# Kernel optimization log

Hardware: AMD Instinct MI355X
Metric: run time of the kernel (lower is better)

The kernel has to match this reference:

```python
import jax, jax.numpy as jnp
import numpy as np

HID = 768
INTER = 3072
H = 12
DH = 64
N = 16384
W = 256   # attention_width
L = 512   # per-sequence length (power of 2, used via the uint32 bit-mask trick)


def rotate_every_two(x):
    x1 = x[..., ::2]
    x2 = x[..., 1::2]
    return jnp.stack((-x2, x1), axis=-1).reshape(x.shape)


def setup_inputs() -> dict:
    key = jax.random.key(0)
    ks = jax.random.split(key, 6)
    # GPT-J style interleaved rotary tables: sin/cos each value repeated twice
    inv_freq = 1.0 / (10000.0 ** (np.arange(0, DH, 2) / DH))  # [DH/2]
    ang = np.arange(N)[:, None] * inv_freq[None, :]           # [N, DH/2]
    pos_sin = jnp.asarray(np.repeat(np.sin(ang), 2, axis=-1), dtype=jnp.float32)
    pos_cos = jnp.asarray(np.repeat(np.cos(ang), 2, axis=-1), dtype=jnp.float32)
    return {
        "x": jax.random.normal(ks[0], (N, HID), dtype=jnp.float32),
        "normed_ages": jax.random.normal(ks[1], (N,), dtype=jnp.float32),
        "pos_sin": pos_sin,
        "pos_cos": pos_cos,
        "ln_scale": jnp.ones((HID,), dtype=jnp.float32),
        "ln_offset": jnp.zeros((HID,), dtype=jnp.float32),
        "w_in": jax.random.normal(ks[2], (HID, 3 * HID + INTER), dtype=jnp.float32) * 0.02,
        "b_in": jnp.zeros((3 * HID + INTER,), dtype=jnp.float32),
        "w_out": jax.random.normal(ks[3], (HID + INTER, HID), dtype=jnp.float32) * 0.02,
        "b_out": jnp.zeros((HID,), dtype=jnp.float32),
        "length": L,
    }


def reference(x, normed_ages, pos_sin, pos_cos, ln_scale, ln_offset,
              w_in, b_in, w_out, b_out, length):
    # LayerNorm (haiku: eps=1e-5, create_scale/offset)
    mu = jnp.mean(x, axis=-1, keepdims=True)
    var = jnp.var(x, axis=-1, keepdims=True)
    xn = (x - mu) * jax.lax.rsqrt(var + 1e-5) * ln_scale + ln_offset

    # fused QKV + FF projection (note: original computes x_with_ages but never uses it)
    mid = xn @ w_in + b_in
    q, k, v, ff = jnp.split(mid, [HID, 2 * HID, 3 * HID], axis=-1)

    def to_heads(t):  # [N, HID] -> [H, N, DH]
        return t.reshape(N, H, DH).transpose(1, 0, 2)

    q, k, v = to_heads(q), to_heads(k), to_heads(v)

    # rotary ('per_head'): sincos broadcast over heads
    sin, cos = pos_sin[None], pos_cos[None]
    q = q * cos + rotate_every_two(q) * sin
    k = k * cos + rotate_every_two(k) * sin

    # local (sliding-window, causal, within-sequence) attention, chunked by W
    C = W
    nc = N // C
    qc = q.reshape(H, nc, C, DH)
    kc = k.reshape(H, nc, C, DH)
    vc = v.reshape(H, nc, C, DH)
    kprev = jnp.concatenate([jnp.zeros_like(kc[:, :1]), kc[:, :-1]], axis=1)
    vprev = jnp.concatenate([jnp.zeros_like(vc[:, :1]), vc[:, :-1]], axis=1)
    kcat = jnp.concatenate([kprev, kc], axis=2)  # [H, nc, 2C, DH]
    vcat = jnp.concatenate([vprev, vc], axis=2)

    qi = (jnp.arange(nc) * C)[:, None] + jnp.arange(C)        # [nc, C]
    kj = (jnp.arange(nc) * C)[:, None] - C + jnp.arange(2 * C)  # [nc, 2C]
    lm = ~(jnp.uint32(length) - jnp.uint32(1))  # same bit-trick as the module
    same_seq = ((qi[:, :, None].astype(jnp.uint32) & lm) ==
                (jnp.maximum(kj, 0)[:, None, :].astype(jnp.uint32) & lm))
    d = qi[:, :, None] - kj[:, None, :]
    mask = (kj[:, None, :] >= 0) & (d >= 0) & (d < W) & same_seq  # [nc, C, 2C]

    scale = 1.0 / jnp.sqrt(jnp.float32(DH))
    scores = jnp.einsum('hncd,hnkd->hnck', qc, kcat) * scale
    scores = jnp.where(mask[None], scores, jnp.float32(-1e30))
    probs = jax.nn.softmax(scores, axis=-1)
    attn = jnp.einsum('hnck,hnkd->hncd', probs, vcat)

    attn = attn.reshape(H, N, DH).transpose(1, 0, 2).reshape(N, HID)
    combined = jnp.concatenate([attn, jax.nn.gelu(ff)], axis=-1)
    return xn + combined @ w_out + b_out
```

## Files before the change

kernel.cpp:

```cpp
#include <hip/hip_runtime.h>

#define N_TOK 16384
#define HIDN  768
#define MIDN  5376
#define COMBN 3840
#define NH    12
#define DHD   64
#define CHUNK 256
#define WIN   256

typedef short s16x8 __attribute__((ext_vector_type(8)));
typedef short s16x4 __attribute__((ext_vector_type(4)));
typedef float f32x4 __attribute__((ext_vector_type(4)));

__device__ __forceinline__ float bf2f(unsigned short u){
  union { unsigned u; float f; } x; x.u = ((unsigned)u) << 16; return x.f;
}
__device__ __forceinline__ unsigned short f2bf(float f){
  union { float f; unsigned u; } x; x.f = f;
  unsigned r = x.u + 0x7fffu + ((x.u >> 16) & 1u);
  return (unsigned short)(r >> 16);
}
__device__ __forceinline__ float gelu_fast(float x){
  float u = -1.5957691216057308f * (x + 0.044715f * x * x * x);
  return x / (1.f + __expf(u));
}
__device__ __forceinline__ void glds16(const void* g, void* l){
  __builtin_amdgcn_global_load_lds(
      (const __attribute__((address_space(1))) unsigned*)g,
      (__attribute__((address_space(3))) unsigned*)l, 16, 0, 0);
}

__global__ __launch_bounds__(256) void transpose_f2b(
    const float* __restrict__ in, unsigned short* __restrict__ out,
    int R, int Cc)
{
  __shared__ short t[64 * 72];
  const int tid = threadIdx.x;
  const int r0 = blockIdx.y * 64, c0 = blockIdx.x * 64;
  #pragma unroll
  for (int rep = 0; rep < 4; rep++){
    int v = tid + 256 * rep;
    int r = v >> 4, s = v & 15;
    float4 d = *(const float4*)(in + (size_t)(r0 + r) * Cc + c0 + s * 4);
    s16x4 o = { (short)f2bf(d.x), (short)f2bf(d.y), (short)f2bf(d.z), (short)f2bf(d.w) };
    *(s16x4*)(t + r * 72 + s * 4) = o;
  }
  __syncthreads();
  #pragma unroll
  for (int rep = 0; rep < 2; rep++){
    int v = tid + 256 * rep;
    int c = v & 63, s2 = v >> 6;
    s16x8 d;
    #pragma unroll
    for (int j = 0; j < 8; j++) d[j] = t[(s2 * 8 + j) * 72 + c];
    *(s16x8*)(out + (size_t)(c0 + c) * R + r0 + s2 * 8) = d;
  }
}

__global__ __launch_bounds__(256) void ln_kernel(
    const float* __restrict__ x, const float* __restrict__ sc,
    const float* __restrict__ ofs, unsigned short* __restrict__ xn)
{
  const int lane = threadIdx.x & 63, wv = threadIdx.x >> 6;
  const int row = blockIdx.x * 4 + wv;
  const float4* xr = (const float4*)(x + (size_t)row * HIDN);
  float4 vals[3];
  float sum = 0.f, sq = 0.f;
  #pragma unroll
  for (int j = 0; j < 3; j++){
    vals[j] = xr[lane + 64 * j];
    sum += vals[j].x + vals[j].y + vals[j].z + vals[j].w;
    sq  += vals[j].x * vals[j].x + vals[j].y * vals[j].y
         + vals[j].z * vals[j].z + vals[j].w * vals[j].w;
  }
  #pragma unroll
  for (int o = 1; o < 64; o <<= 1){ sum += __shfl_xor(sum, o); sq += __shfl_xor(sq, o); }
  const float mu = sum * (1.f / HIDN);
  const float rs = rsqrtf(fmaxf(sq * (1.f / HIDN) - mu * mu, 0.f) + 1e-5f);
  s16x4* xo = (s16x4*)(xn + (size_t)row * HIDN);
  const float4* scp = (const float4*)sc;
  const float4* ofp = (const float4*)ofs;
  #pragma unroll
  for (int j = 0; j < 3; j++){
    int p = lane + 64 * j;
    float4 s = scp[p], o = ofp[p];
    s16x4 w;
    w[0] = (short)f2bf((vals[j].x - mu) * rs * s.x + o.x);
    w[1] = (short)f2bf((vals[j].y - mu) * rs * s.y + o.y);
    w[2] = (short)f2bf((vals[j].z - mu) * rs * s.z + o.z);
    w[3] = (short)f2bf((vals[j].w - mu) * rs * s.w + o.w);
    xo[p] = w;
  }
}

template<int K>
__device__ __forceinline__ void gemm_pipe2(
    const unsigned short* __restrict__ A, const unsigned short* __restrict__ BT,
    short* SM,
    int tid, int quad, int l15, int wr, int wc, int m0, int n0,
    f32x4 acc[4][4])
{
  constexpr int T = K / 64;
  char* const SMc = (char*)SM;
  const int srow = tid >> 2;
  const int ksw  = ((tid & 3) ^ ((tid >> 3) & 3)) * 8;
  const unsigned short* Ap = A  + (size_t)(m0 + srow) * K + ksw;
  const unsigned short* Bp = BT + (size_t)(n0 + srow) * K + ksw;
  const size_t rstep = (size_t)64 * K;

  const int segx = ((quad ^ ((l15 >> 1) & 3)) << 4);
  int offA[4], offB[4];
  #pragma unroll
  for (int mf = 0; mf < 4; mf++) offA[mf] = (wr * 64 + mf * 16 + l15) * 64 + segx;
  #pragma unroll
  for (int nf = 0; nf < 4; nf++) offB[nf] = (wc * 64 + nf * 16 + l15) * 64 + segx;

  auto stage = [&](int tt, int kh, int b){
    const int coff = tt * 64 + kh * 32;
    char* Ad = SMc + b * 32768 + kh * 8192 + tid * 16;
    char* Bd = SMc + b * 32768 + 16384 + kh * 8192 + tid * 16;
    glds16(Ap + coff,         Ad);
    glds16(Ap + coff + rstep, Ad + 4096);
    glds16(Bp + coff,         Bd);
    glds16(Bp + coff + rstep, Bd + 4096);
  };

  s16x8 af[4], bf[4];
  auto rdfrags = [&](int b, int kh){
    const char* Ab = SMc + b * 32768 + kh * 8192;
    const char* Bb = SMc + b * 32768 + 16384 + kh * 8192;
    #pragma unroll
    for (int i = 0; i < 4; i++) af[i] = *(const s16x8*)(Ab + offA[i]);
    #pragma unroll
    for (int j = 0; j < 4; j++) bf[j] = *(const s16x8*)(Bb + offB[j]);
  };

  stage(0, 0, 0);
  stage(0, 1, 0);
  asm volatile("s_waitcnt vmcnt(4)" ::: "memory");
  asm volatile("s_barrier" ::: "memory");
  rdfrags(0, 0);

  for (int t = 0; t < T; ++t){
    const int cur = t & 1;
    if (t + 1 < T) stage(t + 1, 0, cur ^ 1);
    __builtin_amdgcn_s_setprio(1);
    #pragma unroll
    for (int i = 0; i < 4; i++)
      #pragma unroll
      for (int j = 0; j < 4; j++)
        acc[i][j] = __builtin_amdgcn_mfma_f32_16x16x32_bf16(af[i], bf[j], acc[i][j], 0, 0, 0);
    __builtin_amdgcn_s_setprio(0);
    if (t + 1 < T){ asm volatile("s_waitcnt vmcnt(4)" ::: "memory"); }
    else          { asm volatile("s_waitcnt vmcnt(0)" ::: "memory"); }
    asm volatile("s_barrier" ::: "memory");
    rdfrags(cur, 1);
    if (t + 1 < T) stage(t + 1, 1, cur ^ 1);
    __builtin_amdgcn_s_setprio(1);
    #pragma unroll
    for (int i = 0; i < 4; i++)
      #pragma unroll
      for (int j = 0; j < 4; j++)
        acc[i][j] = __builtin_amdgcn_mfma_f32_16x16x32_bf16(af[i], bf[j], acc[i][j], 0, 0, 0);
    __builtin_amdgcn_s_setprio(0);
    if (t + 1 < T){
      asm volatile("s_waitcnt vmcnt(4)" ::: "memory");
      asm volatile("s_barrier" ::: "memory");
      rdfrags(cur ^ 1, 0);
    }
  }
}

__global__ __launch_bounds__(256, 2) void gemm1_k(
    const unsigned short* __restrict__ A, const unsigned short* __restrict__ BT,
    const float* __restrict__ bias,
    unsigned short* __restrict__ qb, unsigned short* __restrict__ kb,
    unsigned short* __restrict__ vb, unsigned short* __restrict__ comb)
{
  __shared__ short SM[32768];
  const int tid = threadIdx.x, lane = tid & 63, wv = tid >> 6;
  const int quad = lane >> 4, l15 = lane & 15;
  const int wr = wv >> 1, wc = wv & 1;

  const int nbx = gridDim.x;
  const int bid = blockIdx.x + blockIdx.y * nbx;
  const int GM = 16;
  const int group = bid / (GM * nbx);
  const int rem   = bid % (GM * nbx);
  const int m0 = (group * GM + (rem % GM)) * 128;
  const int n0 = (rem / GM) * 128;

  f32x4 acc[4][4];
  #pragma unroll
  for (int i = 0; i < 4; i++)
    #pragma unroll
    for (int j = 0; j < 4; j++) acc[i][j] = (f32x4){0.f,0.f,0.f,0.f};

  gemm_pipe2<HIDN>(A, BT, SM, tid, quad, l15, wr, wc, m0, n0, acc);

  unsigned short* dstb; int cb; bool isff = false;
  if (n0 < 768)       { dstb = qb;   cb = n0; }
  else if (n0 < 1536) { dstb = kb;   cb = n0 - 768; }
  else if (n0 < 2304) { dstb = vb;   cb = n0 - 1536; }
  else                { dstb = comb; cb = n0 - 1536; isff = true; }
  const int rowstride = isff ? COMBN : HIDN;

  float bsv[4];
  #pragma unroll
  for (int nf = 0; nf < 4; nf++) bsv[nf] = bias[n0 + wc * 64 + nf * 16 + l15];

  #pragma unroll
  for (int mf = 0; mf < 4; mf++){
    #pragma unroll
    for (int r = 0; r < 4; r++){
      const int row = m0 + wr * 64 + mf * 16 + quad * 4 + r;
      unsigned short* rp = dstb + (size_t)row * rowstride + cb + wc * 64;
      #pragma unroll
      for (int nf = 0; nf < 4; nf++){
        float val = acc[mf][nf][r] + bsv[nf];
        if (isff) val = gelu_fast(val);
        rp[nf * 16 + l15] = f2bf(val);
      }
    }
  }
}

__global__ __launch_bounds__(256, 2) void gemm2_k(
    const unsigned short* __restrict__ A, const unsigned short* __restrict__ BT,
    const float* __restrict__ bias, const unsigned short* __restrict__ xn,
    float* __restrict__ outp)
{
  __shared__ short SM[32768];
  const int tid = threadIdx.x, lane = tid & 63, wv = tid >> 6;
  const int quad = lane >> 4, l15 = lane & 15;
  const int wr = wv >> 1, wc = wv & 1;
  const int n0 = blockIdx.x * 128, m0 = blockIdx.y * 128;

  f32x4 acc[4][4];
  #pragma unroll
  for (int i = 0; i < 4; i++)
    #pragma unroll
    for (int j = 0; j < 4; j++) acc[i][j] = (f32x4){0.f,0.f,0.f,0.f};

  gemm_pipe2<COMBN>(A, BT, SM, tid, quad, l15, wr, wc, m0, n0, acc);

  float bsv[4];
  #pragma unroll
  for (int nf = 0; nf < 4; nf++) bsv[nf] = bias[n0 + wc * 64 + nf * 16 + l15];

  #pragma unroll
  for (int mf = 0; mf < 4; mf++){
    #pragma unroll
    for (int r = 0; r < 4; r++){
      const int row = m0 + wr * 64 + mf * 16 + quad * 4 + r;
      const size_t rb = (size_t)row * HIDN + n0 + wc * 64;
      #pragma unroll
      for (int nf = 0; nf < 4; nf++){
        const size_t o = rb + nf * 16 + l15;
        outp[o] = bf2f(xn[o]) + acc[mf][nf][r] + bsv[nf];
      }
    }
  }
}

__global__ __launch_bounds__(384) void rope_qk(
    unsigned short* __restrict__ qb, unsigned short* __restrict__ kb,
    const float* __restrict__ psin, const float* __restrict__ pcos)
{
  __shared__ float ss[2048], cs[2048];
  const int tid = threadIdx.x, g = blockIdx.x;
  #pragma unroll
  for (int rep = 0; rep < 6; rep++){
    int idx = rep * 384 + tid;
    if (idx < 2048){
      int tok = idx >> 5, p = idx & 31;
      size_t gt = ((size_t)(g * 64 + tok)) * DHD + 2 * p;
      ss[idx] = psin[gt];
      cs[idx] = pcos[gt];
    }
  }
  __syncthreads();
  const int p = tid & 31;
  unsigned* q32 = (unsigned*)qb;
  unsigned* k32 = (unsigned*)kb;
  for (int tok = 0; tok < 64; tok++){
    const size_t a = ((size_t)(g * 64 + tok)) * 384 + tid;
    const float s = ss[tok * 32 + p], c0 = cs[tok * 32 + p];
    unsigned u = q32[a];
    float e = bf2f((unsigned short)(u & 0xffff));
    float d = bf2f((unsigned short)(u >> 16));
    q32[a] = (unsigned)f2bf((e * c0 - d * s) * 0.125f)
           | (((unsigned)f2bf((d * c0 + e * s) * 0.125f)) << 16);
    u = k32[a];
    e = bf2f((unsigned short)(u & 0xffff));
    d = bf2f((unsigned short)(u >> 16));
    k32[a] = (unsigned)f2bf(e * c0 - d * s)
           | (((unsigned)f2bf(d * c0 + e * s)) << 16);
  }
}

__global__ __launch_bounds__(256) void attn_kernel(
    const unsigned short* __restrict__ qb, const unsigned short* __restrict__ kb,
    const unsigned short* __restrict__ vb, unsigned short* __restrict__ comb,
    const int* __restrict__ lenp)
{
  __shared__ short Ks[2][64 * 72];
  __shared__ short Vt[2][64 * 64];
  __shared__ short Ps[4][16 * 72];
  const int tid = threadIdx.x, lane = tid & 63, wv = tid >> 6;
  const int quad = lane >> 4, l15 = lane & 15;
  const int h = blockIdx.y, c = blockIdx.x;
  const unsigned lm = ~((unsigned)lenp[0] - 1u);
  const int i0 = c * CHUNK + wv * 64;
  const unsigned short* qh = qb + h * DHD;
  const unsigned short* kh = kb + h * DHD;
  const unsigned short* vh = vb + h * DHD;

  s16x8 qf[4][2];
  #pragma unroll
  for (int rt = 0; rt < 4; rt++){
    const unsigned short* qr = qh + (size_t)(i0 + rt * 16 + l15) * HIDN;
    qf[rt][0] = *(const s16x8*)(qr + quad * 8);
    qf[rt][1] = *(const s16x8*)(qr + 32 + quad * 8);
  }

  f32x4 O[4][4];
  float mm[4][4], ll[4][4];
  #pragma unroll
  for (int rt = 0; rt < 4; rt++)
    #pragma unroll
    for (int j = 0; j < 4; j++){ O[rt][j] = (f32x4){0,0,0,0}; mm[rt][j] = -1e30f; ll[rt][j] = 0.f; }
  short* myP = &Ps[wv][0];

  const int skey = tid & 63, sseg = tid >> 6;
  const int jb0 = c * CHUNK - 256;
  s16x8 kr[2], vr[2];

  auto issue = [&](int jb){
    if (jb >= 0){
      const unsigned short* kp = kh + (size_t)(jb + skey) * HIDN + sseg * 16;
      const unsigned short* vp = vh + (size_t)(jb + skey) * HIDN + sseg * 16;
      kr[0] = *(const s16x8*)(kp);     kr[1] = *(const s16x8*)(kp + 8);
      vr[0] = *(const s16x8*)(vp);     vr[1] = *(const s16x8*)(vp + 8);
    } else {
      kr[0] = kr[1] = vr[0] = vr[1] = (s16x8){0,0,0,0,0,0,0,0};
    }
  };

  issue(jb0);
  for (int tb = 0; tb < 8; tb++){
    const int jb = jb0 + tb * 64;
    const int buf = tb & 1;
    short* Kb = &Ks[buf][0];
    short* Vb = &Vt[buf][0];
    *(s16x8*)(Kb + skey * 72 + sseg * 16)     = kr[0];
    *(s16x8*)(Kb + skey * 72 + sseg * 16 + 8) = kr[1];
    #pragma unroll
    for (int half = 0; half < 2; half++)
      #pragma unroll
      for (int j = 0; j < 8; j++){
        const int d = sseg * 16 + half * 8 + j;
        Vb[d * 64 + (((skey & 56) ^ ((d & 7) << 3)) | (skey & 7))] = vr[half][j];
      }
    if (tb < 7) issue(jb + 64);
    __syncthreads();

    const bool act = (jb >= 0) && (jb <= i0 + 63) && (jb + 63 >= i0 - 255) &&
                     (((unsigned)i0 & lm) == ((unsigned)jb & lm));
    if (!act) continue;

    #pragma unroll
    for (int rt = 0; rt < 4; rt++){
      const int ilo = i0 + rt * 16;
      if (ilo + 15 < jb || ilo - (jb + 63) >= WIN) continue;
      f32x4 sc[4];
      #pragma unroll
      for (int ct = 0; ct < 4; ct++){
        const short* kbase = Kb + (ct * 16 + l15) * 72 + quad * 8;
        const s16x8 b0 = *(const s16x8*)(kbase);
        const s16x8 b1 = *(const s16x8*)(kbase + 32);
        f32x4 aa = (f32x4){0,0,0,0};
        aa = __builtin_amdgcn_mfma_f32_16x16x32_bf16(qf[rt][0], b0, aa, 0, 0, 0);
        aa = __builtin_amdgcn_mfma_f32_16x16x32_bf16(qf[rt][1], b1, aa, 0, 0, 0);
        sc[ct] = aa;
      }
      float alph[4];
      #pragma unroll
      for (int r = 0; r < 4; r++){
        const int i = ilo + quad * 4 + r;
        #pragma unroll
        for (int ct = 0; ct < 4; ct++){
          const unsigned dd = (unsigned)(i - (jb + ct * 16 + l15));
          if (dd >= 256u) sc[ct][r] = -1e30f;
        }
        float mx = fmaxf(fmaxf(sc[0][r], sc[1][r]), fmaxf(sc[2][r], sc[3][r]));
        mx = fmaxf(mx, __shfl_xor(mx, 1));
        mx = fmaxf(mx, __shfl_xor(mx, 2));
        mx = fmaxf(mx, __shfl_xor(mx, 4));
        mx = fmaxf(mx, __shfl_xor(mx, 8));
        const float mnew = fmaxf(mm[rt][r], mx);
        alph[r] = __expf(mm[rt][r] - mnew);
        mm[rt][r] = mnew;
        float p0 = __expf(sc[0][r] - mnew);
        float p1 = __expf(sc[1][r] - mnew);
        float p2 = __expf(sc[2][r] - mnew);
        float p3 = __expf(sc[3][r] - mnew);
        sc[0][r] = p0; sc[1][r] = p1; sc[2][r] = p2; sc[3][r] = p3;
        float rsum = (p0 + p1) + (p2 + p3);
        rsum += __shfl_xor(rsum, 1);
        rsum += __shfl_xor(rsum, 2);
        rsum += __shfl_xor(rsum, 4);
        rsum += __shfl_xor(rsum, 8);
        ll[rt][r] = ll[rt][r] * alph[r] + rsum;
      }
      #pragma unroll
      for (int co = 0; co < 4; co++)
        #pragma unroll
        for (int r = 0; r < 4; r++) O[rt][co][r] *= alph[r];
      #pragma unroll
      for (int r = 0; r < 4; r++){
        const int prow = quad * 4 + r;
        #pragma unroll
        for (int ct = 0; ct < 4; ct++)
          myP[prow * 72 + ct * 16 + l15] = (short)f2bf(sc[ct][r]);
      }
      #pragma unroll
      for (int ks2 = 0; ks2 < 2; ks2++){
        const s16x8 pf = *(const s16x8*)(myP + l15 * 72 + ks2 * 32 + quad * 8);
        #pragma unroll
        for (int co = 0; co < 4; co++){
          const int d = co * 16 + l15;
          const s16x8 vf = *(const s16x8*)(Vb + d * 64 +
                              ((ks2 * 32 + quad * 8) ^ ((d & 7) << 3)));
          O[rt][co] = __builtin_amdgcn_mfma_f32_16x16x32_bf16(pf, vf, O[rt][co], 0, 0, 0);
        }
      }
    }
  }

  #pragma unroll
  for (int rt = 0; rt < 4; rt++)
    #pragma unroll
    for (int co = 0; co < 4; co++)
      #pragma unroll
      for (int r = 0; r < 4; r++){
        const int tok = i0 + rt * 16 + quad * 4 + r;
        comb[(size_t)tok * COMBN + h * DHD + co * 16 + l15] = f2bf(O[rt][co][r] / ll[rt][r]);
      }
}

extern "C" void kernel_launch(void* const* d_in, const int* in_sizes, int n_in,
                              void* d_out, int out_size, void* d_ws, size_t ws_size,
                              hipStream_t stream)
{
  const float* x     = (const float*)d_in[0];
  const float* psin  = (const float*)d_in[2];
  const float* pcos  = (const float*)d_in[3];
  const float* lns   = (const float*)d_in[4];
  const float* lno   = (const float*)d_in[5];
  const float* w_in  = (const float*)d_in[6];
  const float* b_in  = (const float*)d_in[7];
  const float* w_out = (const float*)d_in[8];
  const float* b_out = (const float*)d_in[9];
  const int*   lenp  = (const int*)d_in[10];
  float* out = (float*)d_out;

  char* ws = (char*)d_ws;
  size_t off = 0;
  unsigned short* xn    = (unsigned short*)(ws + off); off += (size_t)N_TOK * HIDN * 2;
  unsigned short* wInT  = (unsigned short*)(ws + off); off += (size_t)MIDN * HIDN * 2;
  unsigned short* wOutT = (unsigned short*)(ws + off); off += (size_t)HIDN * COMBN * 2;
  unsigned short* qbuf  = (unsigned short*)(ws + off); off += (size_t)N_TOK * HIDN * 2;
  unsigned short* kbuf  = (unsigned short*)(ws + off); off += (size_t)N_TOK * HIDN * 2;
  unsigned short* vbuf  = (unsigned short*)(ws + off); off += (size_t)N_TOK * HIDN * 2;
  unsigned short* comb  = (unsigned short*)(ws + off); off += (size_t)N_TOK * COMBN * 2;

  transpose_f2b<<<dim3(MIDN/64, HIDN/64), 256, 0, stream>>>(w_in, wInT, HIDN, MIDN);
  transpose_f2b<<<dim3(HIDN/64, COMBN/64), 256, 0, stream>>>(w_out, wOutT, COMBN, HIDN);
  ln_kernel<<<dim3(N_TOK/4), 256, 0, stream>>>(x, lns, lno, xn);
  gemm1_k<<<dim3(MIDN/128, N_TOK/128), 256, 0, stream>>>(
      xn, wInT, b_in, qbuf, kbuf, vbuf, comb);
  rope_qk<<<dim3(N_TOK/64), 384, 0, stream>>>(qbuf, kbuf, psin, pcos);
  attn_kernel<<<dim3(N_TOK/CHUNK, NH), 256, 0, stream>>>(
      qbuf, kbuf, vbuf, comb, lenp);
  gemm2_k<<<dim3(HIDN/128, N_TOK/128), 256, 0, stream>>>(
      comb, wOutT, b_out, xn, out);
}
```

Before: 613.7 us.

## Fuse rotary embedding into QKV GEMM epilogue and remap tiles per XCD

The rotary embedding and the query scaling now run inside the first GEMM's epilogue, using a lane shuffle to fetch each pair partner. This removes the separate rope kernel and its extra read and write pass over the q and k buffers. The block-to-tile mapping also changes so that consecutive block IDs (round-robin across the 8 XCDs) land on a contiguous group of M tiles per XCD, aiming for better L2 reuse. The epilogue now reads sin/cos tables directly from global memory, which adds some load traffic and register pressure.

```diff
diff --git a/kernel.cpp b/kernel.cpp
--- a/kernel.cpp
+++ b/kernel.cpp
@@ -175,6 +175,7 @@
 __global__ __launch_bounds__(256, 2) void gemm1_k(
     const unsigned short* __restrict__ A, const unsigned short* __restrict__ BT,
     const float* __restrict__ bias,
+    const float* __restrict__ psin, const float* __restrict__ pcos,
     unsigned short* __restrict__ qb, unsigned short* __restrict__ kb,
     unsigned short* __restrict__ vb, unsigned short* __restrict__ comb)
 {
@@ -183,13 +184,10 @@
   const int quad = lane >> 4, l15 = lane & 15;
   const int wr = wv >> 1, wc = wv & 1;
 
-  const int nbx = gridDim.x;
-  const int bid = blockIdx.x + blockIdx.y * nbx;
-  const int GM = 16;
-  const int group = bid / (GM * nbx);
-  const int rem   = bid % (GM * nbx);
-  const int m0 = (group * GM + (rem % GM)) * 128;
-  const int n0 = (rem / GM) * 128;
+  const int p = blockIdx.x + blockIdx.y * gridDim.x;
+  const int xcd = p & 7, slot = p >> 3;
+  const int m0 = (xcd * 16 + (slot & 15)) * 128;
+  const int n0 = (slot >> 4) * 128;
 
   f32x4 acc[4][4];
   #pragma unroll
@@ -199,28 +197,51 @@
 
   gemm_pipe2<HIDN>(A, BT, SM, tid, quad, l15, wr, wc, m0, n0, acc);
 
-  unsigned short* dstb; int cb; bool isff = false;
-  if (n0 < 768)       { dstb = qb;   cb = n0; }
-  else if (n0 < 1536) { dstb = kb;   cb = n0 - 768; }
-  else if (n0 < 2304) { dstb = vb;   cb = n0 - 1536; }
-  else                { dstb = comb; cb = n0 - 1536; isff = true; }
-  const int rowstride = isff ? COMBN : HIDN;
+  unsigned short* dstb; int cb; int cls;
+  if (n0 < 768)       { dstb = qb;   cb = n0;        cls = 0; }
+  else if (n0 < 1536) { dstb = kb;   cb = n0 - 768;  cls = 1; }
+  else if (n0 < 2304) { dstb = vb;   cb = n0 - 1536; cls = 2; }
+  else                { dstb = comb; cb = n0 - 1536; cls = 3; }
+  const int rowstride = (cls == 3) ? COMBN : HIDN;
 
   float bsv[4];
   #pragma unroll
   for (int nf = 0; nf < 4; nf++) bsv[nf] = bias[n0 + wc * 64 + nf * 16 + l15];
 
-  #pragma unroll
-  for (int mf = 0; mf < 4; mf++){
-    #pragma unroll
-    for (int r = 0; r < 4; r++){
-      const int row = m0 + wr * 64 + mf * 16 + quad * 4 + r;
-      unsigned short* rp = dstb + (size_t)row * rowstride + cb + wc * 64;
-      #pragma unroll
-      for (int nf = 0; nf < 4; nf++){
-        float val = acc[mf][nf][r] + bsv[nf];
-        if (isff) val = gelu_fast(val);
-        rp[nf * 16 + l15] = f2bf(val);
+  if (cls <= 1){
+    const float qscale = (cls == 0) ? 0.125f : 1.0f;
+    #pragma unroll
+    for (int mf = 0; mf < 4; mf++){
+      #pragma unroll
+      for (int r = 0; r < 4; r++){
+        const int row = m0 + wr * 64 + mf * 16 + quad * 4 + r;
+        unsigned short* rp = dstb + (size_t)row * rowstride + cb + wc * 64;
+        const float* sp = psin + (size_t)row * DHD;
+        const float* cp = pcos + (size_t)row * DHD;
+        #pragma unroll
+        for (int nf = 0; nf < 4; nf++){
+          const int d = nf * 16 + l15;
+          float v = acc[mf][nf][r] + bsv[nf];
+          float vp = __shfl_xor(v, 1);
+          const float s = sp[d], c = cp[d];
+          float o = (l15 & 1) ? (v * c + vp * s) : (v * c - vp * s);
+          rp[d] = f2bf(o * qscale);
+        }
+      }
+    }
+  } else {
+    #pragma unroll
+    for (int mf = 0; mf < 4; mf++){
+      #pragma unroll
+      for (int r = 0; r < 4; r++){
+        const int row = m0 + wr * 64 + mf * 16 + quad * 4 + r;
+        unsigned short* rp = dstb + (size_t)row * rowstride + cb + wc * 64;
+        #pragma unroll
+        for (int nf = 0; nf < 4; nf++){
+          float val = acc[mf][nf][r] + bsv[nf];
+          if (cls == 3) val = gelu_fast(val);
+          rp[nf * 16 + l15] = f2bf(val);
+        }
       }
     }
   }
@@ -261,42 +282,6 @@
         outp[o] = bf2f(xn[o]) + acc[mf][nf][r] + bsv[nf];
       }
     }
-  }
-}
-
-__global__ __launch_bounds__(384) void rope_qk(
-    unsigned short* __restrict__ qb, unsigned short* __restrict__ kb,
-    const float* __restrict__ psin, const float* __restrict__ pcos)
-{
-  __shared__ float ss[2048], cs[2048];
-  const int tid = threadIdx.x, g = blockIdx.x;
-  #pragma unroll
-  for (int rep = 0; rep < 6; rep++){
-    int idx = rep * 384 + tid;
-    if (idx < 2048){
-      int tok = idx >> 5, p = idx & 31;
-      size_t gt = ((size_t)(g * 64 + tok)) * DHD + 2 * p;
-      ss[idx] = psin[gt];
-      cs[idx] = pcos[gt];
-    }
-  }
-  __syncthreads();
-  const int p = tid & 31;
-  unsigned* q32 = (unsigned*)qb;
-  unsigned* k32 = (unsigned*)kb;
-  for (int tok = 0; tok < 64; tok++){
-    const size_t a = ((size_t)(g * 64 + tok)) * 384 + tid;
-    const float s = ss[tok * 32 + p], c0 = cs[tok * 32 + p];
-    unsigned u = q32[a];
-    float e = bf2f((unsigned short)(u & 0xffff));
-    float d = bf2f((unsigned short)(u >> 16));
-    q32[a] = (unsigned)f2bf((e * c0 - d * s) * 0.125f)
-           | (((unsigned)f2bf((d * c0 + e * s) * 0.125f)) << 16);
-    u = k32[a];
-    e = bf2f((unsigned short)(u & 0xffff));
-    d = bf2f((unsigned short)(u >> 16));
-    k32[a] = (unsigned)f2bf(e * c0 - d * s)
-           | (((unsigned)f2bf(d * c0 + e * s)) << 16);
   }
 }
 
@@ -480,8 +465,7 @@
   transpose_f2b<<<dim3(HIDN/64, COMBN/64), 256, 0, stream>>>(w_out, wOutT, COMBN, HIDN);
   ln_kernel<<<dim3(N_TOK/4), 256, 0, stream>>>(x, lns, lno, xn);
   gemm1_k<<<dim3(MIDN/128, N_TOK/128), 256, 0, stream>>>(
-      xn, wInT, b_in, qbuf, kbuf, vbuf, comb);
-  rope_qk<<<dim3(N_TOK/64), 384, 0, stream>>>(qbuf, kbuf, psin, pcos);
+      xn, wInT, b_in, psin, pcos, qbuf, kbuf, vbuf, comb);
   attn_kernel<<<dim3(N_TOK/CHUNK, NH), 256, 0, stream>>>(
       qbuf, kbuf, vbuf, comb, lenp);
   gemm2_k<<<dim3(HIDN/128, N_TOK/128), 256, 0, stream>>>(
```

After: 608.2 us. Within noise of the previous version (-0.9%).
